# Kernel tuning notes

Measured on AMD Instinct MI355X. Metric: run time of the kernel, lower is better.

## Reference

```python
import jax, jax.numpy as jnp
import numpy as np

NEG_SLOPE = 0.2


def gatv2(x, src, dst, eattr, Wl, bl, Wr, br, We, att, bias, concat):
    # GATv2Conv (PyG semantics): message j->i, softmax over incoming edges of target i.
    n = x.shape[0]
    H, C = att.shape
    xl = (x @ Wl + bl).reshape(n, H, C)   # source transform lin_l
    xr = (x @ Wr + br).reshape(n, H, C)   # target transform lin_r
    xe = (eattr @ We).reshape(-1, H, C)   # edge transform lin_edge (no bias)
    g = jax.nn.leaky_relu(xl[src] + xr[dst] + xe, NEG_SLOPE)  # [E,H,C]
    e = jnp.einsum('ehc,hc->eh', g, att)                      # [E,H]
    m = jax.ops.segment_max(e, dst, num_segments=n)
    a = jnp.exp(e - m[dst])
    s = jax.ops.segment_sum(a, dst, num_segments=n)
    alpha = a / (s[dst] + 1e-16)                              # [E,H]
    out = jax.ops.segment_sum(alpha[:, :, None] * xl[src], dst, num_segments=n)
    out = out.reshape(n, H * C) if concat else out.mean(axis=1)
    return out + bias, alpha


def add_self_loops(src, dst, eattr, n):
    # PyG default: add_self_loops=True, fill_value='mean' for edge_attr
    loop = jnp.arange(n, dtype=src.dtype)
    fill = jnp.broadcast_to(eattr.mean(axis=0, keepdims=True), (n, eattr.shape[1]))
    return (jnp.concatenate([src, loop]), jnp.concatenate([dst, loop]),
            jnp.concatenate([eattr, fill], axis=0))


def setup_inputs() -> dict:
    key = jax.random.key(0)
    ks = iter(jax.random.split(key, 64))
    B, N, D = 4, 2048, 256
    n = B * N
    E = 131072
    H, C1 = 4, 64  # conv1: heads=4, out=hidden//heads=64 (concat -> 256)
    C2 = 256       # conv2: heads=4, out=256, concat=False (mean)
    IN1 = 770

    def rn(shape, s=0.05):
        return jax.random.normal(next(ks), shape, dtype=jnp.float32) * s

    inp = {
        'h': rn((B, N, D), 1.0), 'c_temp': rn((B, N, D), 1.0),
        'c_stereo': rn((B, N, D), 1.0), 'e_proj': rn((B, N, 2), 1.0),
        'f_Lt': rn((B, N, D), 1.0),
        'edges': jax.random.randint(next(ks), (2, E), 0, n, dtype=jnp.int64),
        'edge_attr': rn((E, 1), 1.0),
        # conv1
        'Wl1': rn((IN1, H * C1)), 'bl1': jnp.zeros((H * C1,), jnp.float32),
        'Wr1': rn((IN1, H * C1)), 'br1': jnp.zeros((H * C1,), jnp.float32),
        'We1': rn((1, H * C1)), 'att1': rn((H, C1)),
        'bias1': jnp.zeros((H * C1,), jnp.float32),
        # conv2
        'Wl2': rn((D, H * C2)), 'bl2': jnp.zeros((H * C2,), jnp.float32),
        'Wr2': rn((D, H * C2)), 'br2': jnp.zeros((H * C2,), jnp.float32),
        'We2': rn((1, H * C2)), 'att2': rn((H, C2)),
        'bias2': jnp.zeros((C2,), jnp.float32),
        # GRUCell ([in, 3H] layout; gate order r,z,n as in torch)
        'Wih': rn((D, 3 * D)), 'bih': jnp.zeros((3 * D,), jnp.float32),
        'Whh': rn((D, 3 * D)), 'bhh': jnp.zeros((3 * D,), jnp.float32),
        # heads
        'rW1': rn((D, 256)), 'rb1': jnp.zeros((256,), jnp.float32),
        'rW2': rn((256, 2)), 'rb2': jnp.zeros((2,), jnp.float32),
        'wW1': rn((D, 256)), 'wb1': jnp.zeros((256,), jnp.float32),
        'wW2': rn((256, 2)), 'wb2': jnp.zeros((2,), jnp.float32),
        'pW1': rn((D, 128)), 'pb1': jnp.zeros((128,), jnp.float32),
        'pW2': rn((128, 1)), 'pb2': jnp.zeros((1,), jnp.float32),
        'dW1': rn((D, 128)), 'db1': jnp.zeros((128,), jnp.float32),
        'dW2': rn((128, 1)), 'db2': jnp.zeros((1,), jnp.float32),
    }
    return inp


def reference(h, c_temp, c_stereo, e_proj, f_Lt, edges, edge_attr,
              Wl1, bl1, Wr1, br1, We1, att1, bias1,
              Wl2, bl2, Wr2, br2, We2, att2, bias2,
              Wih, bih, Whh, bhh,
              rW1, rb1, rW2, rb2, wW1, wb1, wW2, wb2,
              pW1, pb1, pW2, pb2, dW1, db1, dW2, db2):
    B, N, D = f_Lt.shape
    n = B * N
    x = jnp.concatenate([c_temp, c_stereo, e_proj, f_Lt], axis=-1).reshape(n, -1)

    src, dst, ea = add_self_loops(edges[0], edges[1], edge_attr, n)
    x1, _ = gatv2(x, src, dst, ea, Wl1, bl1, Wr1, br1, We1, att1, bias1, concat=True)
    x1 = jax.nn.relu(x1)
    x2, alpha = gatv2(x1, src, dst, ea, Wl2, bl2, Wr2, br2, We2, att2, bias2, concat=False)

    # GRUCell
    hf = h.reshape(n, -1)
    gi = x2 @ Wih + bih
    gh = hf @ Whh + bhh
    ir, iz, inew = jnp.split(gi, 3, axis=-1)
    hr, hz, hnew = jnp.split(gh, 3, axis=-1)
    r_g = jax.nn.sigmoid(ir + hr)
    z_g = jax.nn.sigmoid(iz + hz)
    n_g = jnp.tanh(inew + r_g * hnew)
    h_new = ((1.0 - z_g) * n_g + z_g * hf).reshape(B, N, D)

    res = jax.nn.relu(h_new @ rW1 + rb1) @ rW2 + rb2
    w = jax.nn.sigmoid(jax.nn.relu(h_new @ wW1 + wb1) @ wW2 + wb2)
    a_p = jax.nn.softplus(jax.nn.relu(h_new @ pW1 + pb1) @ pW2 + pb2).mean(axis=1)
    a_d = jax.nn.softplus(jax.nn.relu(h_new @ dW1 + db1) @ dW2 + db2)
    return (h_new, res, w, a_p, a_d)
```

## Files before the change

kernel.cpp:

```cpp
#include <hip/hip_runtime.h>
#include <hip/hip_bf16.h>
#include <cstdint>
#include <cstddef>

#define N_NODES 8192
#define E_RAW   131072
#define E_TOT   (E_RAW + N_NODES)
#define HEADS   4

typedef __attribute__((ext_vector_type(8))) __bf16 bf16x8;
typedef __attribute__((ext_vector_type(4))) float f32x4;

__device__ __forceinline__ void gload_lds16(const void* g, void* lds) {
  __builtin_amdgcn_global_load_lds(
      (const __attribute__((address_space(1))) unsigned int*)g,
      (__attribute__((address_space(3))) unsigned int*)lds, 16, 0, 0);
}

__device__ __forceinline__ float bfbits2f(unsigned short u) {
  return __uint_as_float((unsigned)u << 16);
}
__device__ __forceinline__ unsigned short f2bfbits(float f) {
  __hip_bfloat16 b = __float2bfloat16(f);
  return *(unsigned short*)&b;
}
__device__ __forceinline__ void unpk(unsigned u, float& lo, float& hi) {
  lo = __uint_as_float(u << 16);
  hi = __uint_as_float(u & 0xffff0000u);
}

__device__ __forceinline__ int eSrc(const int* __restrict__ src, int e) {
  return (e < E_RAW) ? src[e] : (e - E_RAW);
}
__device__ __forceinline__ int eDst(const int* __restrict__ dst, int e) {
  return (e < E_RAW) ? dst[e] : (e - E_RAW);
}


__global__ __launch_bounds__(256) void prep_kernel(
    const float* __restrict__ ct, const float* __restrict__ cs,
    const float* __restrict__ ep, const float* __restrict__ fl,
    const float* __restrict__ h, const float* __restrict__ ea,
    const float* bl1, const float* br1, const float* bl2, const float* br2,
    const float* rb1, const float* wb1, const float* pb1, const float* db1,
    __hip_bfloat16* __restrict__ x, __hip_bfloat16* __restrict__ Hb,
    float* __restrict__ MP, int* __restrict__ icnt_ipos,
    float* B1, float* B2, float* BH) {
  int blk = blockIdx.x;
  int tid = threadIdx.x;
  if (blk < 8192) {
    int i = blk;
    for (int j = tid; j < 832; j += 256) {
      float v;
      if (j < 256)      v = ct[(size_t)i * 256 + j];
      else if (j < 512) v = cs[(size_t)i * 256 + (j - 256)];
      else if (j < 514) v = ep[(size_t)i * 2 + (j - 512)];
      else if (j < 770) v = fl[(size_t)i * 256 + (j - 514)];
      else              v = 0.f;
      x[(size_t)i * 832 + j] = __float2bfloat16(v);
    }
  } else if (blk < 9216) {
    size_t base = ((size_t)(blk - 8192) * 256 + tid) * 8;
    float4 a = *(const float4*)(h + base);
    float4 b = *(const float4*)(h + base + 4);
    unsigned short o[8];
    o[0]=f2bfbits(a.x); o[1]=f2bfbits(a.y); o[2]=f2bfbits(a.z); o[3]=f2bfbits(a.w);
    o[4]=f2bfbits(b.x); o[5]=f2bfbits(b.y); o[6]=f2bfbits(b.z); o[7]=f2bfbits(b.w);
    *(uint4*)((unsigned short*)Hb + base) = *(uint4*)o;
  } else if (blk < 9472) {
    __shared__ float sm[256];
    int bb = blk - 9216;
    float acc = 0.f;
    for (int i = bb * 256 + tid; i < E_RAW; i += 256 * 256) acc += ea[i];
    sm[tid] = acc; __syncthreads();
    for (int s = 128; s; s >>= 1) { if (tid < s) sm[tid] += sm[tid + s]; __syncthreads(); }
    if (tid == 0) MP[bb] = sm[0];
  } else if (blk < 9536) {
    int i = (blk - 9472) * 256 + tid;
    if (i < 2 * N_NODES) icnt_ipos[i] = 0;
  } else {
    int i = (blk - 9536) * 256 + tid;
    if (i < 512) B1[i] = (i < 256) ? bl1[i] : br1[i - 256];
    else if (i < 2560) { int k = i - 512; B2[k] = (k < 1024) ? bl2[k] : br2[k - 1024]; }
    else if (i < 3328) {
      int k = i - 2560;
      BH[k] = (k < 256) ? rb1[k] : (k < 512) ? wb1[k - 256] : (k < 640) ? pb1[k - 512] : db1[k - 640];
    }
  }
}


__global__ void csr_count(const int* __restrict__ dst, int* __restrict__ cnt) {
  int e = blockIdx.x * blockDim.x + threadIdx.x;
  if (e < E_TOT) atomicAdd(&cnt[eDst(dst, e)], 1);
}

__global__ __launch_bounds__(1024) void csr_scan(const int* __restrict__ cnt,
                                                 int* __restrict__ off,
                                                 float* __restrict__ MP) {
  __shared__ int part[1024];
  __shared__ float sm[256];
  int t = threadIdx.x;
  if (t < 256) sm[t] = MP[t];
  __syncthreads();
  for (int s = 128; s; s >>= 1) { if (t < s) sm[t] += sm[t + s]; __syncthreads(); }
  if (t == 0) MP[256] = sm[0] * (1.f / (float)E_RAW);
  int base = t * 8;
  int loc[8];
  int s = 0;
#pragma unroll
  for (int i = 0; i < 8; ++i) { loc[i] = s; s += cnt[base + i]; }
  part[t] = s; __syncthreads();
  for (int d = 1; d < 1024; d <<= 1) {
    int v = (t >= d) ? part[t - d] : 0;
    __syncthreads();
    part[t] += v;
    __syncthreads();
  }
  int pre = (t == 0) ? 0 : part[t - 1];
#pragma unroll
  for (int i = 0; i < 8; ++i) off[base + i] = pre + loc[i];
  if (t == 1023) off[8192] = part[1023];
}

__global__ void csr_fill(const int* __restrict__ src, const int* __restrict__ dst,
                         const float* __restrict__ ea, const float* __restrict__ eamean,
                         const int* __restrict__ off, int* __restrict__ pos,
                         int* __restrict__ srcn, float* __restrict__ eav) {
  int e = blockIdx.x * blockDim.x + threadIdx.x;
  if (e >= E_TOT) return;
  int d = eDst(dst, e);
  int p = off[d] + atomicAdd(&pos[d], 1);
  srcn[p] = eSrc(src, e);
  eav[p] = (e < E_RAW) ? ea[e] : eamean[0];
}


__global__ __launch_bounds__(256) void wt_all(
    const float* w0, const float* w1, const float* w2, const float* w3,
    const float* w4, const float* w5, const float* w6, const float* w7,
    const float* w8, const float* w9,
    __hip_bfloat16* WT1, __hip_bfloat16* WT2, __hip_bfloat16* WTih,
    __hip_bfloat16* WThh, __hip_bfloat16* WTh) {
  const int cum[10] = {208, 416, 672, 928, 1120, 1312, 1376, 1440, 1472, 1504};
  const int Kt[10]  = {770, 770, 256, 256, 256, 256, 256, 256, 256, 256};
  const int Nt[10]  = {256, 256, 1024, 1024, 768, 768, 256, 256, 128, 128};
  const int KPt[10] = {832, 832, 256, 256, 256, 256, 256, 256, 256, 256};
  const int n0t[10] = {0, 256, 0, 1024, 0, 0, 0, 256, 512, 640};
  int job = 0;
  while (blockIdx.x >= (unsigned)cum[job]) ++job;
  int lb = blockIdx.x - (job ? cum[job - 1] : 0);
  int K = Kt[job], N = Nt[job], KP = KPt[job], n0 = n0t[job];
  int tilesX = KP >> 5;
  int k0 = (lb % tilesX) * 32, nb = (lb / tilesX) * 32;
  const float* W;
  switch (job) {
    case 0: W = w0; break; case 1: W = w1; break; case 2: W = w2; break;
    case 3: W = w3; break; case 4: W = w4; break; case 5: W = w5; break;
    case 6: W = w6; break; case 7: W = w7; break; case 8: W = w8; break;
    default: W = w9; break;
  }
  __hip_bfloat16* WT = (job < 2) ? WT1 : (job < 4) ? WT2 : (job == 4) ? WTih
                       : (job == 5) ? WThh : WTh;
  __shared__ float sm[32][33];
  int tx = threadIdx.x & 31, ty = threadIdx.x >> 5;
  for (int yy = ty; yy < 32; yy += 8) {
    int k = k0 + yy, n = nb + tx;
    sm[yy][tx] = (k < K && n < N) ? W[(size_t)k * N + n] : 0.f;
  }
  __syncthreads();
  for (int yy = ty; yy < 32; yy += 8) {
    int n = nb + yy, k = k0 + tx;
    if (n < N) WT[(size_t)(n0 + n) * KP + k] = __float2bfloat16(sm[tx][yy]);
  }
}


template <int OUT>
__global__ __launch_bounds__(256) void mfma_gemm(
    const __hip_bfloat16* __restrict__ A, const __hip_bfloat16* __restrict__ BT,
    const float* __restrict__ bias, void* __restrict__ Cout, int KP, int N,
    const __hip_bfloat16* A2, const __hip_bfloat16* BT2,
    const float* bias2, void* C2) {
  if (blockIdx.z == 1) { A = A2; BT = BT2; bias = bias2; Cout = C2; }
  __shared__ uint4 AsBuf[1024];
  __shared__ uint4 BsBuf[1024];
  char* Asc = (char*)AsBuf;
  char* Bsc = (char*)BsBuf;
  int tid = threadIdx.x;
  int lane = tid & 63;
  int wid = tid >> 6;
  int wr = wid >> 1, wc = wid & 1;
  int bm = blockIdx.y * 128;
  int bn = blockIdx.x * 128;
  f32x4 acc[4][4];
#pragma unroll
  for (int i = 0; i < 4; ++i)
#pragma unroll
    for (int j = 0; j < 4; ++j) acc[i][j] = (f32x4){0.f, 0.f, 0.f, 0.f};

  int nK = KP >> 6;
  for (int kt = 0; kt < nK; ++kt) {
    int k0 = kt * 64;
#pragma unroll
    for (int i = 0; i < 4; ++i) {
      int p = i * 256 + tid;
      int row = p >> 3, cc = p & 7;
      int sc = cc ^ (row & 7);
      gload_lds16(A + (size_t)(bm + row) * KP + k0 + sc * 8, Asc + p * 16);
      gload_lds16(BT + (size_t)(bn + row) * KP + k0 + sc * 8, Bsc + p * 16);
    }
    __syncthreads();
#pragma unroll
    for (int s = 0; s < 2; ++s) {
      bf16x8 af[4], bfr[4];
#pragma unroll
      for (int f = 0; f < 4; ++f) {
        int r = wr * 64 + f * 16 + (lane & 15);
        int ch = (s * 4 + (lane >> 4)) ^ (r & 7);
        af[f] = *(const bf16x8*)(Asc + r * 128 + ch * 16);
        int n = wc * 64 + f * 16 + (lane & 15);
        int cb = (s * 4 + (lane >> 4)) ^ (n & 7);
        bfr[f] = *(const bf16x8*)(Bsc + n * 128 + cb * 16);
      }
#pragma unroll
      for (int fm = 0; fm < 4; ++fm)
#pragma unroll
        for (int fn = 0; fn < 4; ++fn)
          acc[fm][fn] = __builtin_amdgcn_mfma_f32_16x16x32_bf16(af[fm], bfr[fn], acc[fm][fn], 0, 0, 0);
    }
    __syncthreads();
  }
  int rbase = bm + wr * 64 + (lane >> 4) * 4;
  int cbase = bn + wc * 64 + (lane & 15);
#pragma unroll
  for (int fm = 0; fm < 4; ++fm)
#pragma unroll
    for (int fn = 0; fn < 4; ++fn) {
      int col = cbase + fn * 16;
      float bv = bias[col];
#pragma unroll
      for (int j = 0; j < 4; ++j) {
        int row = rbase + fm * 16 + j;
        float v = acc[fm][fn][j] + bv;
        if (OUT == 2 || OUT == 3) v = fmaxf(v, 0.f);
        if (OUT == 0 || OUT == 3)
          ((__hip_bfloat16*)Cout)[(size_t)row * N + col] = __float2bfloat16(v);
        else
          ((float*)Cout)[(size_t)row * N + col] = v;
      }
    }
}


__global__ __launch_bounds__(256, 4) void gat_fused1(
    const __hip_bfloat16* __restrict__ XLR,
    const int* __restrict__ off, const int* __restrict__ srcn,
    const float* __restrict__ eav, const float* __restrict__ We,
    const float* __restrict__ att, const float* __restrict__ bias,
    __hip_bfloat16* __restrict__ X1) {
  __shared__ float lds_a[4][256];
  __shared__ float sm_m[4][4], sm_ss[4][4], sst[4];
  int d = blockIdx.x;
  int tid = threadIdx.x;
  int w = tid >> 6, lane = tid & 63;
  int g = lane >> 4, q = lane & 15;
  int j0 = g * 64 + q * 4;
  const unsigned short* X = (const unsigned short*)XLR;
  ushort4 xrv = *(const ushort4*)(X + (size_t)d * 512 + 256 + j0);
  float xr[4] = {bfbits2f(xrv.x), bfbits2f(xrv.y), bfbits2f(xrv.z), bfbits2f(xrv.w)};
  float4 wev = *(const float4*)(We + j0);
  float4 atv = *(const float4*)(att + j0);
  float we[4] = {wev.x, wev.y, wev.z, wev.w};
  float at[4] = {atv.x, atv.y, atv.z, atv.w};
  int b = off[d], deg = off[d + 1] - b;
  int nw = (deg > w) ? ((deg - w + 3) >> 2) : 0;
  float m = -INFINITY, ss = 0.f;
  float a[4] = {0.f, 0.f, 0.f, 0.f};
  if (nw > 0) {
    int p0 = b + w;
    int pe = p0 + 4 * (nw - 1);
    int sB = srcn[p0]; float eaA = eav[p0];
    ushort4 vvA = *(const ushort4*)(X + (size_t)sB * 512 + j0);
    int p1 = min(p0 + 4, pe);
    sB = srcn[p1]; float eaB = eav[p1];
    for (int k = 0; k < nw; ++k) {
      ushort4 vv = vvA; float ea = eaA;
      eaA = eaB;
      vvA = *(const ushort4*)(X + (size_t)sB * 512 + j0);
      int p2 = min(p0 + 4 * (k + 2), pe);
      sB = srcn[p2]; eaB = eav[p2];
      float v[4] = {bfbits2f(vv.x), bfbits2f(vv.y), bfbits2f(vv.z), bfbits2f(vv.w)};
      float t = 0.f;
#pragma unroll
      for (int i = 0; i < 4; ++i) {
        float gg = fmaf(ea, we[i], v[i] + xr[i]);
        float lr = fmaxf(gg, 0.2f * gg);
        t = fmaf(lr, at[i], t);
      }
      t += __shfl_xor(t, 8, 64); t += __shfl_xor(t, 4, 64);
      t += __shfl_xor(t, 2, 64); t += __shfl_xor(t, 1, 64);
      if (__all(t <= m)) {
        float wp = __expf(t - m);
        ss += wp;
#pragma unroll
        for (int i = 0; i < 4; ++i) a[i] = fmaf(wp, v[i], a[i]);
      } else {
        float mn = fmaxf(m, t);
        float scl = __expf(m - mn);
        float wp = __expf(t - mn);
        ss = fmaf(ss, scl, wp);
#pragma unroll
        for (int i = 0; i < 4; ++i) a[i] = fmaf(wp, v[i], a[i] * scl);
        m = mn;
      }
    }
  }
  if (q == 0) { sm_m[w][g] = m; sm_ss[w][g] = ss; }
  __syncthreads();
  float M = fmaxf(fmaxf(sm_m[0][g], sm_m[1][g]), fmaxf(sm_m[2][g], sm_m[3][g]));
  float scale = __expf(m - M);
#pragma unroll
  for (int i = 0; i < 4; ++i) lds_a[w][j0 + i] = a[i] * scale;
  if (w == 0 && q == 0) {
    float st = 1e-16f;
#pragma unroll
    for (int ww = 0; ww < 4; ++ww) st += sm_ss[ww][g] * __expf(sm_m[ww][g] - M);
    sst[g] = st;
  }
  __syncthreads();
  int c = tid;
  float val = lds_a[0][c] + lds_a[1][c] + lds_a[2][c] + lds_a[3][c];
  float outv = val / sst[c >> 6] + bias[c];
  X1[(size_t)d * 256 + c] = __float2bfloat16(fmaxf(outv, 0.f));
}


__global__ __launch_bounds__(256, 4) void gat_fused2(
    const __hip_bfloat16* __restrict__ XLR,
    const int* __restrict__ off, const int* __restrict__ srcn,
    const float* __restrict__ eav, const float* __restrict__ We,
    const float* __restrict__ att, const float* __restrict__ bias,
    __hip_bfloat16* __restrict__ X2) {
  __shared__ float lds_a[4][1024];
  __shared__ float sm_m[4][4], sm_ss[4][4], sst[4];
  int d = blockIdx.x;
  int tid = threadIdx.x;
  int w = tid >> 6, lane = tid & 63;
  int g = lane >> 4, q = lane & 15;
  int j0 = g * 256 + q * 16;
  const unsigned short* X = (const unsigned short*)XLR;
  float xr[16], we[16], at[16];
  {
    const uint4* xp = (const uint4*)(X + (size_t)d * 2048 + 1024 + j0);
    uint4 r0 = xp[0], r1 = xp[1];
    unpk(r0.x, xr[0], xr[1]); unpk(r0.y, xr[2], xr[3]);
    unpk(r0.z, xr[4], xr[5]); unpk(r0.w, xr[6], xr[7]);
    unpk(r1.x, xr[8], xr[9]); unpk(r1.y, xr[10], xr[11]);
    unpk(r1.z, xr[12], xr[13]); unpk(r1.w, xr[14], xr[15]);
#pragma unroll
    for (int i = 0; i < 16; i += 4) {
      float4 w4 = *(const float4*)(We + j0 + i);
      float4 a4 = *(const float4*)(att + j0 + i);
      we[i] = w4.x; we[i + 1] = w4.y; we[i + 2] = w4.z; we[i + 3] = w4.w;
      at[i] = a4.x; at[i + 1] = a4.y; at[i + 2] = a4.z; at[i + 3] = a4.w;
    }
  }
  int b = off[d], deg = off[d + 1] - b;
  int nw = (deg > w) ? ((deg - w + 3) >> 2) : 0;
  float m = -INFINITY, ss = 0.f;
  float a[16];
#pragma unroll
  for (int i = 0; i < 16; ++i) a[i] = 0.f;
  if (nw > 0) {
    int p0 = b + w;
    int pe = p0 + 4 * (nw - 1);
    int sB = srcn[p0]; float eaA = eav[p0];
    const uint4* rp = (const uint4*)(X + (size_t)sB * 2048 + j0);
    uint4 rA0 = rp[0], rA1 = rp[1];
    int p1 = min(p0 + 4, pe);
    sB = srcn[p1]; float eaB = eav[p1];
    for (int k = 0; k < nw; ++k) {
      uint4 c0 = rA0, c1 = rA1; float ea = eaA;
      eaA = eaB;
      rp = (const uint4*)(X + (size_t)sB * 2048 + j0);
      rA0 = rp[0]; rA1 = rp[1];
      int p2 = min(p0 + 4 * (k + 2), pe);
      sB = srcn[p2]; eaB = eav[p2];
      float v[16];
      unpk(c0.x, v[0], v[1]); unpk(c0.y, v[2], v[3]);
      unpk(c0.z, v[4], v[5]); unpk(c0.w, v[6], v[7]);
      unpk(c1.x, v[8], v[9]); unpk(c1.y, v[10], v[11]);
      unpk(c1.z, v[12], v[13]); unpk(c1.w, v[14], v[15]);
      float t = 0.f;
#pragma unroll
      for (int i = 0; i < 16; ++i) {
        float gg = fmaf(ea, we[i], v[i] + xr[i]);
        float lr = fmaxf(gg, 0.2f * gg);
        t = fmaf(lr, at[i], t);
      }
      t += __shfl_xor(t, 8, 64); t += __shfl_xor(t, 4, 64);
      t += __shfl_xor(t, 2, 64); t += __shfl_xor(t, 1, 64);
      if (__all(t <= m)) {
        float wp = __expf(t - m);
        ss += wp;
#pragma unroll
        for (int i = 0; i < 16; ++i) a[i] = fmaf(wp, v[i], a[i]);
      } else {
        float mn = fmaxf(m, t);
        float scl = __expf(m - mn);
        float wp = __expf(t - mn);
        ss = fmaf(ss, scl, wp);
#pragma unroll
        for (int i = 0; i < 16; ++i) a[i] = fmaf(wp, v[i], a[i] * scl);
        m = mn;
      }
    }
  }
  if (q == 0) { sm_m[w][g] = m; sm_ss[w][g] = ss; }
  __syncthreads();
  float M = fmaxf(fmaxf(sm_m[0][g], sm_m[1][g]), fmaxf(sm_m[2][g], sm_m[3][g]));
  float scale = __expf(m - M);
#pragma unroll
  for (int i = 0; i < 16; ++i) {
    int ir = (i + q) & 15;
    lds_a[w][j0 + ir] = a[ir] * scale;
  }
  if (w == 0 && q == 0) {
    float st = 1e-16f;
#pragma unroll
    for (int ww = 0; ww < 4; ++ww) st += sm_ss[ww][g] * __expf(sm_m[ww][g] - M);
    sst[g] = st;
  }
  __syncthreads();
  int c = tid;
  float acc = 0.f;
#pragma unroll
  for (int hh = 0; hh < 4; ++hh) {
    int addr = hh * 256 + c;
    float sv = lds_a[0][addr] + lds_a[1][addr] + lds_a[2][addr] + lds_a[3][addr];
    acc += sv / sst[hh];
  }
  X2[(size_t)d * 256 + c] = __float2bfloat16(fmaf(0.25f, acc, bias[c]));
}


__global__ void gru_kernel(const __hip_bfloat16* __restrict__ gi,
                           const __hip_bfloat16* __restrict__ gh,
                           const float* __restrict__ hf, float* __restrict__ hn,
                           __hip_bfloat16* __restrict__ hnb) {
  int i = blockIdx.x;
  int c = threadIdx.x;
  size_t b = (size_t)i * 768;
  const unsigned short* giu = (const unsigned short*)gi;
  const unsigned short* ghu = (const unsigned short*)gh;
  float ir = bfbits2f(giu[b + c]), iz = bfbits2f(giu[b + 256 + c]), in_ = bfbits2f(giu[b + 512 + c]);
  float hr = bfbits2f(ghu[b + c]), hz = bfbits2f(ghu[b + 256 + c]), hn_ = bfbits2f(ghu[b + 512 + c]);
  float r = 1.f / (1.f + __expf(-(ir + hr)));
  float z = 1.f / (1.f + __expf(-(iz + hz)));
  float ng = tanhf(in_ + r * hn_);
  float h0 = hf[(size_t)i * 256 + c];
  float v = (1.f - z) * ng + z * h0;
  hn[(size_t)i * 256 + c] = v;
  hnb[(size_t)i * 256 + c] = __float2bfloat16(v);
}


__global__ __launch_bounds__(256) void heads_final(
    const __hip_bfloat16* __restrict__ Tb,
    const float* __restrict__ rW2, const float* __restrict__ rb2,
    const float* __restrict__ wW2, const float* __restrict__ wb2,
    const float* __restrict__ pW2, const float* __restrict__ pb2,
    const float* __restrict__ dW2, const float* __restrict__ db2,
    float* __restrict__ o_res, float* __restrict__ o_w,
    float* __restrict__ AP, float* __restrict__ o_ad) {
  int node = (blockIdx.x * 256 + threadIdx.x) >> 6;
  int lane = threadIdx.x & 63;
  const unsigned short* t = (const unsigned short*)Tb + (size_t)node * 768;
  ushort4 tr = *(const ushort4*)(t + lane * 4);
  ushort4 tw = *(const ushort4*)(t + 256 + lane * 4);
  float trf[4] = {bfbits2f(tr.x), bfbits2f(tr.y), bfbits2f(tr.z), bfbits2f(tr.w)};
  float twf[4] = {bfbits2f(tw.x), bfbits2f(tw.y), bfbits2f(tw.z), bfbits2f(tw.w)};
  float tpf[4] = {0.f, 0.f, 0.f, 0.f}, tdf[4] = {0.f, 0.f, 0.f, 0.f};
  if (lane < 32) {
    ushort4 tp = *(const ushort4*)(t + 512 + lane * 4);
    ushort4 td = *(const ushort4*)(t + 640 + lane * 4);
    tpf[0] = bfbits2f(tp.x); tpf[1] = bfbits2f(tp.y); tpf[2] = bfbits2f(tp.z); tpf[3] = bfbits2f(tp.w);
    tdf[0] = bfbits2f(td.x); tdf[1] = bfbits2f(td.y); tdf[2] = bfbits2f(td.z); tdf[3] = bfbits2f(td.w);
  }
  float r0 = 0.f, r1 = 0.f, w0 = 0.f, w1 = 0.f, pp = 0.f, dd = 0.f;
#pragma unroll
  for (int i = 0; i < 4; ++i) {
    int k = lane * 4 + i;
    r0 = fmaf(trf[i], rW2[k * 2], r0);
    r1 = fmaf(trf[i], rW2[k * 2 + 1], r1);
    w0 = fmaf(twf[i], wW2[k * 2], w0);
    w1 = fmaf(twf[i], wW2[k * 2 + 1], w1);
  }
  if (lane < 32) {
#pragma unroll
    for (int i = 0; i < 4; ++i) {
      int k = lane * 4 + i;
      pp = fmaf(tpf[i], pW2[k], pp);
      dd = fmaf(tdf[i], dW2[k], dd);
    }
  }
#pragma unroll
  for (int o = 32; o; o >>= 1) {
    r0 += __shfl_xor(r0, o, 64); r1 += __shfl_xor(r1, o, 64);
    w0 += __shfl_xor(w0, o, 64); w1 += __shfl_xor(w1, o, 64);
    pp += __shfl_xor(pp, o, 64); dd += __shfl_xor(dd, o, 64);
  }
  if (lane == 0) {
    o_res[(size_t)node * 2]     = r0 + rb2[0];
    o_res[(size_t)node * 2 + 1] = r1 + rb2[1];
    float sw0 = w0 + wb2[0], sw1 = w1 + wb2[1];
    o_w[(size_t)node * 2]     = 1.f / (1.f + __expf(-sw0));
    o_w[(size_t)node * 2 + 1] = 1.f / (1.f + __expf(-sw1));
    float vp = pp + pb2[0];
    AP[node] = fmaxf(vp, 0.f) + log1pf(__expf(-fabsf(vp)));
    float vd = dd + db2[0];
    o_ad[node] = fmaxf(vd, 0.f) + log1pf(__expf(-fabsf(vd)));
  }
}

__global__ void ap_reduce(const float* __restrict__ ap, float* __restrict__ out) {
  __shared__ float sm[256];
  int b = blockIdx.x, tid = threadIdx.x;
  float acc = 0.f;
  for (int i = tid; i < 2048; i += 256) acc += ap[b * 2048 + i];
  sm[tid] = acc; __syncthreads();
  for (int s = 128; s; s >>= 1) { if (tid < s) sm[tid] += sm[tid + s]; __syncthreads(); }
  if (tid == 0) out[b] = sm[0] * (1.f / 2048.f);
}


extern "C" void kernel_launch(void* const* d_in, const int* in_sizes, int n_in,
                              void* d_out, int out_size, void* d_ws, size_t ws_size,
                              hipStream_t stream) {
  const float* h        = (const float*)d_in[0];
  const float* c_temp   = (const float*)d_in[1];
  const float* c_stereo = (const float*)d_in[2];
  const float* e_proj   = (const float*)d_in[3];
  const float* f_Lt     = (const float*)d_in[4];
  const int*   edges    = (const int*)d_in[5];
  const float* eattr    = (const float*)d_in[6];
  const float* Wl1 = (const float*)d_in[7];  const float* bl1 = (const float*)d_in[8];
  const float* Wr1 = (const float*)d_in[9];  const float* br1 = (const float*)d_in[10];
  const float* We1 = (const float*)d_in[11]; const float* att1 = (const float*)d_in[12];
  const float* bias1 = (const float*)d_in[13];
  const float* Wl2 = (const float*)d_in[14]; const float* bl2 = (const float*)d_in[15];
  const float* Wr2 = (const float*)d_in[16]; const float* br2 = (const float*)d_in[17];
  const float* We2 = (const float*)d_in[18]; const float* att2 = (const float*)d_in[19];
  const float* bias2 = (const float*)d_in[20];
  const float* Wih = (const float*)d_in[21]; const float* bih = (const float*)d_in[22];
  const float* Whh = (const float*)d_in[23]; const float* bhh = (const float*)d_in[24];
  const float* rW1 = (const float*)d_in[25]; const float* rb1 = (const float*)d_in[26];
  const float* rW2 = (const float*)d_in[27]; const float* rb2 = (const float*)d_in[28];
  const float* wW1 = (const float*)d_in[29]; const float* wb1 = (const float*)d_in[30];
  const float* wW2 = (const float*)d_in[31]; const float* wb2 = (const float*)d_in[32];
  const float* pW1 = (const float*)d_in[33]; const float* pb1 = (const float*)d_in[34];
  const float* pW2 = (const float*)d_in[35]; const float* pb2 = (const float*)d_in[36];
  const float* dW1 = (const float*)d_in[37]; const float* db1 = (const float*)d_in[38];
  const float* dW2 = (const float*)d_in[39]; const float* db2 = (const float*)d_in[40];

  const int* src = edges;
  const int* dst = edges + E_RAW;

  float* base = (float*)d_ws;
  size_t cur = 0;
  auto alloc = [&](size_t n) { float* p = base + cur; cur += (n + 63) & ~(size_t)63; return p; };

  float* BIG0 = alloc(8388608);
  float* BIG1 = alloc(6291456);
  float* XLR1f = alloc(2097152);
  float* X1f  = alloc(1048576);
  float* X2f  = alloc(1048576);
  float* Hbf  = alloc(1048576);
  float* HNbf = alloc(1048576);
  float* WT1f = alloc(212992);
  float* WT2f = alloc(262144);
  float* WTihf = alloc(98304);
  float* WThhf = alloc(98304);
  float* WThf  = alloc(98304);
  float* B1 = alloc(512);
  float* B2 = alloc(2048);
  float* BH = alloc(768);
  float* EAV = alloc(E_TOT);
  float* AP  = alloc(N_NODES);
  float* MP  = alloc(320);
  int* ICNT = (int*)alloc(2 * N_NODES);
  int* IOFF = (int*)alloc(N_NODES + 64);
  int* ISRC = (int*)alloc(E_TOT);
  if (ws_size < cur * 4) return;
  int* IPOS = ICNT + N_NODES;

  __hip_bfloat16* x_bf = (__hip_bfloat16*)BIG1;
  __hip_bfloat16* XLR1 = (__hip_bfloat16*)XLR1f;
  __hip_bfloat16* XLR2 = (__hip_bfloat16*)BIG0;
  __hip_bfloat16* X1b = (__hip_bfloat16*)X1f;
  __hip_bfloat16* X2b = (__hip_bfloat16*)X2f;
  __hip_bfloat16* Hb  = (__hip_bfloat16*)Hbf;
  __hip_bfloat16* HNb = (__hip_bfloat16*)HNbf;
  __hip_bfloat16* WT1 = (__hip_bfloat16*)WT1f;
  __hip_bfloat16* WT2 = (__hip_bfloat16*)WT2f;
  __hip_bfloat16* WTih = (__hip_bfloat16*)WTihf;
  __hip_bfloat16* WThh = (__hip_bfloat16*)WThhf;
  __hip_bfloat16* WTh  = (__hip_bfloat16*)WThf;
  __hip_bfloat16* gi = (__hip_bfloat16*)BIG0;
  __hip_bfloat16* gh = (__hip_bfloat16*)BIG1;
  __hip_bfloat16* Tb = (__hip_bfloat16*)BIG0;

  float* o_hnew = (float*)d_out;
  float* o_res  = o_hnew + (size_t)N_NODES * 256;
  float* o_w    = o_res + (size_t)N_NODES * 2;
  float* o_ap   = o_w + (size_t)N_NODES * 2;
  float* o_ad   = o_ap + 4;

  prep_kernel<<<9549, 256, 0, stream>>>(c_temp, c_stereo, e_proj, f_Lt, h, eattr,
                                        bl1, br1, bl2, br2, rb1, wb1, pb1, db1,
                                        x_bf, Hb, MP, ICNT, B1, B2, BH);
  csr_count<<<(E_TOT + 255) / 256, 256, 0, stream>>>(dst, ICNT);
  csr_scan<<<1, 1024, 0, stream>>>(ICNT, IOFF, MP);
  csr_fill<<<(E_TOT + 255) / 256, 256, 0, stream>>>(src, dst, eattr, MP + 256,
                                                    IOFF, IPOS, ISRC, EAV);
  wt_all<<<1504, 256, 0, stream>>>(Wl1, Wr1, Wl2, Wr2, Wih, Whh, rW1, wW1, pW1, dW1,
                                   WT1, WT2, WTih, WThh, WTh);

  mfma_gemm<0><<<dim3(4, 64, 1), 256, 0, stream>>>(x_bf, WT1, B1, XLR1, 832, 512,
                                                   nullptr, nullptr, nullptr, nullptr);
  gat_fused1<<<N_NODES, 256, 0, stream>>>(XLR1, IOFF, ISRC, EAV, We1, att1, bias1, X1b);

  mfma_gemm<0><<<dim3(16, 64, 1), 256, 0, stream>>>(X1b, WT2, B2, XLR2, 256, 2048,
                                                    nullptr, nullptr, nullptr, nullptr);
  gat_fused2<<<N_NODES, 256, 0, stream>>>(XLR2, IOFF, ISRC, EAV, We2, att2, bias2, X2b);

  mfma_gemm<0><<<dim3(6, 64, 2), 256, 0, stream>>>(X2b, WTih, bih, gi, 256, 768,
                                                   Hb, WThh, bhh, gh);
  gru_kernel<<<N_NODES, 256, 0, stream>>>(gi, gh, h, o_hnew, HNb);

  mfma_gemm<3><<<dim3(6, 64, 1), 256, 0, stream>>>(HNb, WTh, BH, Tb, 256, 768,
                                                   nullptr, nullptr, nullptr, nullptr);
  heads_final<<<N_NODES / 4, 256, 0, stream>>>(Tb, rW2, rb2, wW2, wb2, pW2, pb2, dW2, db2,
                                               o_res, o_w, AP, o_ad);
  ap_reduce<<<4, 256, 0, stream>>>(AP, o_ap);
}
```

Before: 229.0 us.

## Assign one wave per head in GAT aggregation kernels instead of splitting edges

Both GAT aggregation kernels now give each wavefront one attention head and have it walk every incoming edge of the node sequentially. Previously the four waves split the edges and each lane group covered all heads. This removes the cross-wave online-softmax merge (shared max/sum exchange and one barrier) and cuts per-thread register arrays from 16 to 4 floats in the second layer. In exchange, each wave now runs the full-degree loop, lengthening the serial dependency chain per block. The per-edge score reduction also grows from four to six shuffles, and the occupancy hint in the launch bounds is dropped.

Result: slower. 254.0 us (+10.9%).

```diff
diff --git a/kernel.cpp b/kernel.cpp
--- a/kernel.cpp
+++ b/kernel.cpp
@@ -253,195 +253,114 @@
 }
 
 
-__global__ __launch_bounds__(256, 4) void gat_fused1(
+__global__ __launch_bounds__(256) void gat_fused1(
     const __hip_bfloat16* __restrict__ XLR,
     const int* __restrict__ off, const int* __restrict__ srcn,
     const float* __restrict__ eav, const float* __restrict__ We,
     const float* __restrict__ att, const float* __restrict__ bias,
     __hip_bfloat16* __restrict__ X1) {
-  __shared__ float lds_a[4][256];
-  __shared__ float sm_m[4][4], sm_ss[4][4], sst[4];
   int d = blockIdx.x;
-  int tid = threadIdx.x;
-  int w = tid >> 6, lane = tid & 63;
-  int g = lane >> 4, q = lane & 15;
-  int j0 = g * 64 + q * 4;
+  int w = threadIdx.x >> 6;
+  int lane = threadIdx.x & 63;
+  int j0 = w * 64 + lane;
   const unsigned short* X = (const unsigned short*)XLR;
-  ushort4 xrv = *(const ushort4*)(X + (size_t)d * 512 + 256 + j0);
+  float xr = bfbits2f(X[(size_t)d * 512 + 256 + j0]);
+  float we = We[j0], at = att[j0];
+  int b = off[d], e1 = off[d + 1], pe = e1 - 1;
+  int sB = srcn[b]; float eaA = eav[b];
+  unsigned short vA = X[(size_t)sB * 512 + j0];
+  int p1 = min(b + 1, pe); sB = srcn[p1]; float eaB = eav[p1];
+  float m = -INFINITY, ss = 0.f, a = 0.f;
+  for (int p = b; p < e1; ++p) {
+    unsigned short vu = vA; float ea = eaA; eaA = eaB;
+    vA = X[(size_t)sB * 512 + j0];
+    int p2 = min(p + 2, pe); sB = srcn[p2]; eaB = eav[p2];
+    float v = bfbits2f(vu);
+    float gg = fmaf(ea, we, v + xr);
+    float lr = fmaxf(gg, 0.2f * gg);
+    float t = lr * at;
+    t += __shfl_xor(t, 32, 64); t += __shfl_xor(t, 16, 64);
+    t += __shfl_xor(t, 8, 64);  t += __shfl_xor(t, 4, 64);
+    t += __shfl_xor(t, 2, 64);  t += __shfl_xor(t, 1, 64);
+    if (__all(t <= m)) {
+      float wp = __expf(t - m);
+      ss += wp;
+      a = fmaf(wp, v, a);
+    } else {
+      float mn = fmaxf(m, t);
+      float scl = __expf(m - mn);
+      float wp = __expf(t - mn);
+      ss = fmaf(ss, scl, wp);
+      a = fmaf(wp, v, a * scl);
+      m = mn;
+    }
+  }
+  float outv = a / (ss + 1e-16f) + bias[j0];
+  ((unsigned short*)X1)[(size_t)d * 256 + j0] = f2bfbits(fmaxf(outv, 0.f));
+}
+
+
+__global__ __launch_bounds__(256) void gat_fused2(
+    const __hip_bfloat16* __restrict__ XLR,
+    const int* __restrict__ off, const int* __restrict__ srcn,
+    const float* __restrict__ eav, const float* __restrict__ We,
+    const float* __restrict__ att, const float* __restrict__ bias,
+    __hip_bfloat16* __restrict__ X2) {
+  __shared__ float hacc[4][256];
+  int d = blockIdx.x;
+  int w = threadIdx.x >> 6;
+  int lane = threadIdx.x & 63;
+  int j0 = w * 256 + lane * 4;
+  const unsigned short* X = (const unsigned short*)XLR;
+  ushort4 xrv = *(const ushort4*)(X + (size_t)d * 2048 + 1024 + j0);
   float xr[4] = {bfbits2f(xrv.x), bfbits2f(xrv.y), bfbits2f(xrv.z), bfbits2f(xrv.w)};
   float4 wev = *(const float4*)(We + j0);
   float4 atv = *(const float4*)(att + j0);
   float we[4] = {wev.x, wev.y, wev.z, wev.w};
   float at[4] = {atv.x, atv.y, atv.z, atv.w};
-  int b = off[d], deg = off[d + 1] - b;
-  int nw = (deg > w) ? ((deg - w + 3) >> 2) : 0;
+  int b = off[d], e1 = off[d + 1], pe = e1 - 1;
+  int sB = srcn[b]; float eaA = eav[b];
+  ushort4 vvA = *(const ushort4*)(X + (size_t)sB * 2048 + j0);
+  int p1 = min(b + 1, pe); sB = srcn[p1]; float eaB = eav[p1];
   float m = -INFINITY, ss = 0.f;
   float a[4] = {0.f, 0.f, 0.f, 0.f};
-  if (nw > 0) {
-    int p0 = b + w;
-    int pe = p0 + 4 * (nw - 1);
-    int sB = srcn[p0]; float eaA = eav[p0];
-    ushort4 vvA = *(const ushort4*)(X + (size_t)sB * 512 + j0);
-    int p1 = min(p0 + 4, pe);
-    sB = srcn[p1]; float eaB = eav[p1];
-    for (int k = 0; k < nw; ++k) {
-      ushort4 vv = vvA; float ea = eaA;
-      eaA = eaB;
-      vvA = *(const ushort4*)(X + (size_t)sB * 512 + j0);
-      int p2 = min(p0 + 4 * (k + 2), pe);
-      sB = srcn[p2]; eaB = eav[p2];
-      float v[4] = {bfbits2f(vv.x), bfbits2f(vv.y), bfbits2f(vv.z), bfbits2f(vv.w)};
-      float t = 0.f;
-#pragma unroll
-      for (int i = 0; i < 4; ++i) {
-        float gg = fmaf(ea, we[i], v[i] + xr[i]);
-        float lr = fmaxf(gg, 0.2f * gg);
-        t = fmaf(lr, at[i], t);
-      }
-      t += __shfl_xor(t, 8, 64); t += __shfl_xor(t, 4, 64);
-      t += __shfl_xor(t, 2, 64); t += __shfl_xor(t, 1, 64);
-      if (__all(t <= m)) {
-        float wp = __expf(t - m);
-        ss += wp;
-#pragma unroll
-        for (int i = 0; i < 4; ++i) a[i] = fmaf(wp, v[i], a[i]);
-      } else {
-        float mn = fmaxf(m, t);
-        float scl = __expf(m - mn);
-        float wp = __expf(t - mn);
-        ss = fmaf(ss, scl, wp);
-#pragma unroll
-        for (int i = 0; i < 4; ++i) a[i] = fmaf(wp, v[i], a[i] * scl);
-        m = mn;
-      }
-    }
-  }
-  if (q == 0) { sm_m[w][g] = m; sm_ss[w][g] = ss; }
+  for (int p = b; p < e1; ++p) {
+    ushort4 vv = vvA; float ea = eaA; eaA = eaB;
+    vvA = *(const ushort4*)(X + (size_t)sB * 2048 + j0);
+    int p2 = min(p + 2, pe); sB = srcn[p2]; eaB = eav[p2];
+    float v[4] = {bfbits2f(vv.x), bfbits2f(vv.y), bfbits2f(vv.z), bfbits2f(vv.w)};
+    float t = 0.f;
+#pragma unroll
+    for (int i = 0; i < 4; ++i) {
+      float gg = fmaf(ea, we[i], v[i] + xr[i]);
+      float lr = fmaxf(gg, 0.2f * gg);
+      t = fmaf(lr, at[i], t);
+    }
+    t += __shfl_xor(t, 32, 64); t += __shfl_xor(t, 16, 64);
+    t += __shfl_xor(t, 8, 64);  t += __shfl_xor(t, 4, 64);
+    t += __shfl_xor(t, 2, 64);  t += __shfl_xor(t, 1, 64);
+    if (__all(t <= m)) {
+      float wp = __expf(t - m);
+      ss += wp;
+#pragma unroll
+      for (int i = 0; i < 4; ++i) a[i] = fmaf(wp, v[i], a[i]);
+    } else {
+      float mn = fmaxf(m, t);
+      float scl = __expf(m - mn);
+      float wp = __expf(t - mn);
+      ss = fmaf(ss, scl, wp);
+#pragma unroll
+      for (int i = 0; i < 4; ++i) a[i] = fmaf(wp, v[i], a[i] * scl);
+      m = mn;
+    }
+  }
+  float inv = 1.f / (ss + 1e-16f);
+#pragma unroll
+  for (int i = 0; i < 4; ++i) hacc[w][lane * 4 + i] = a[i] * inv;
   __syncthreads();
-  float M = fmaxf(fmaxf(sm_m[0][g], sm_m[1][g]), fmaxf(sm_m[2][g], sm_m[3][g]));
-  float scale = __expf(m - M);
-#pragma unroll
-  for (int i = 0; i < 4; ++i) lds_a[w][j0 + i] = a[i] * scale;
-  if (w == 0 && q == 0) {
-    float st = 1e-16f;
-#pragma unroll
-    for (int ww = 0; ww < 4; ++ww) st += sm_ss[ww][g] * __expf(sm_m[ww][g] - M);
-    sst[g] = st;
-  }
-  __syncthreads();
-  int c = tid;
-  float val = lds_a[0][c] + lds_a[1][c] + lds_a[2][c] + lds_a[3][c];
-  float outv = val / sst[c >> 6] + bias[c];
-  X1[(size_t)d * 256 + c] = __float2bfloat16(fmaxf(outv, 0.f));
-}
-
-
-__global__ __launch_bounds__(256, 4) void gat_fused2(
-    const __hip_bfloat16* __restrict__ XLR,
-    const int* __restrict__ off, const int* __restrict__ srcn,
-    const float* __restrict__ eav, const float* __restrict__ We,
-    const float* __restrict__ att, const float* __restrict__ bias,
-    __hip_bfloat16* __restrict__ X2) {
-  __shared__ float lds_a[4][1024];
-  __shared__ float sm_m[4][4], sm_ss[4][4], sst[4];
-  int d = blockIdx.x;
-  int tid = threadIdx.x;
-  int w = tid >> 6, lane = tid & 63;
-  int g = lane >> 4, q = lane & 15;
-  int j0 = g * 256 + q * 16;
-  const unsigned short* X = (const unsigned short*)XLR;
-  float xr[16], we[16], at[16];
-  {
-    const uint4* xp = (const uint4*)(X + (size_t)d * 2048 + 1024 + j0);
-    uint4 r0 = xp[0], r1 = xp[1];
-    unpk(r0.x, xr[0], xr[1]); unpk(r0.y, xr[2], xr[3]);
-    unpk(r0.z, xr[4], xr[5]); unpk(r0.w, xr[6], xr[7]);
-    unpk(r1.x, xr[8], xr[9]); unpk(r1.y, xr[10], xr[11]);
-    unpk(r1.z, xr[12], xr[13]); unpk(r1.w, xr[14], xr[15]);
-#pragma unroll
-    for (int i = 0; i < 16; i += 4) {
-      float4 w4 = *(const float4*)(We + j0 + i);
-      float4 a4 = *(const float4*)(att + j0 + i);
-      we[i] = w4.x; we[i + 1] = w4.y; we[i + 2] = w4.z; we[i + 3] = w4.w;
-      at[i] = a4.x; at[i + 1] = a4.y; at[i + 2] = a4.z; at[i + 3] = a4.w;
-    }
-  }
-  int b = off[d], deg = off[d + 1] - b;
-  int nw = (deg > w) ? ((deg - w + 3) >> 2) : 0;
-  float m = -INFINITY, ss = 0.f;
-  float a[16];
-#pragma unroll
-  for (int i = 0; i < 16; ++i) a[i] = 0.f;
-  if (nw > 0) {
-    int p0 = b + w;
-    int pe = p0 + 4 * (nw - 1);
-    int sB = srcn[p0]; float eaA = eav[p0];
-    const uint4* rp = (const uint4*)(X + (size_t)sB * 2048 + j0);
-    uint4 rA0 = rp[0], rA1 = rp[1];
-    int p1 = min(p0 + 4, pe);
-    sB = srcn[p1]; float eaB = eav[p1];
-    for (int k = 0; k < nw; ++k) {
-      uint4 c0 = rA0, c1 = rA1; float ea = eaA;
-      eaA = eaB;
-      rp = (const uint4*)(X + (size_t)sB * 2048 + j0);
-      rA0 = rp[0]; rA1 = rp[1];
-      int p2 = min(p0 + 4 * (k + 2), pe);
-      sB = srcn[p2]; eaB = eav[p2];
-      float v[16];
-      unpk(c0.x, v[0], v[1]); unpk(c0.y, v[2], v[3]);
-      unpk(c0.z, v[4], v[5]); unpk(c0.w, v[6], v[7]);
-      unpk(c1.x, v[8], v[9]); unpk(c1.y, v[10], v[11]);
-      unpk(c1.z, v[12], v[13]); unpk(c1.w, v[14], v[15]);
-      float t = 0.f;
-#pragma unroll
-      for (int i = 0; i < 16; ++i) {
-        float gg = fmaf(ea, we[i], v[i] + xr[i]);
-        float lr = fmaxf(gg, 0.2f * gg);
-        t = fmaf(lr, at[i], t);
-      }
-      t += __shfl_xor(t, 8, 64); t += __shfl_xor(t, 4, 64);
-      t += __shfl_xor(t, 2, 64); t += __shfl_xor(t, 1, 64);
-      if (__all(t <= m)) {
-        float wp = __expf(t - m);
-        ss += wp;
-#pragma unroll
-        for (int i = 0; i < 16; ++i) a[i] = fmaf(wp, v[i], a[i]);
-      } else {
-        float mn = fmaxf(m, t);
-        float scl = __expf(m - mn);
-        float wp = __expf(t - mn);
-        ss = fmaf(ss, scl, wp);
-#pragma unroll
-        for (int i = 0; i < 16; ++i) a[i] = fmaf(wp, v[i], a[i] * scl);
-        m = mn;
-      }
-    }
-  }
-  if (q == 0) { sm_m[w][g] = m; sm_ss[w][g] = ss; }
-  __syncthreads();
-  float M = fmaxf(fmaxf(sm_m[0][g], sm_m[1][g]), fmaxf(sm_m[2][g], sm_m[3][g]));
-  float scale = __expf(m - M);
-#pragma unroll
-  for (int i = 0; i < 16; ++i) {
-    int ir = (i + q) & 15;
-    lds_a[w][j0 + ir] = a[ir] * scale;
-  }
-  if (w == 0 && q == 0) {
-    float st = 1e-16f;
-#pragma unroll
-    for (int ww = 0; ww < 4; ++ww) st += sm_ss[ww][g] * __expf(sm_m[ww][g] - M);
-    sst[g] = st;
-  }
-  __syncthreads();
-  int c = tid;
-  float acc = 0.f;
-#pragma unroll
-  for (int hh = 0; hh < 4; ++hh) {
-    int addr = hh * 256 + c;
-    float sv = lds_a[0][addr] + lds_a[1][addr] + lds_a[2][addr] + lds_a[3][addr];
-    acc += sv / sst[hh];
-  }
-  X2[(size_t)d * 256 + c] = __float2bfloat16(fmaf(0.25f, acc, bias[c]));
+  int c = threadIdx.x;
+  float ov = 0.25f * (hacc[0][c] + hacc[1][c] + hacc[2][c] + hacc[3][c]) + bias[c];
+  X2[(size_t)d * 256 + c] = __float2bfloat16(ov);
 }
 
 
```
